# Performance work log

Hardware: AMD Instinct MI355X
Metric: run time of the kernel (lower is better)

Reference implementation:

```python
import jax, jax.numpy as jnp
import numpy as np

B, N, D, E, R = 2, 50000, 128, 500000, 500
LN_EPS = 1e-5


def setup_inputs() -> dict:
    key = jax.random.key(0)
    ks = jax.random.split(key, 12)
    s = 1.0 / np.sqrt(D)
    s2 = 1.0 / np.sqrt(2 * D)
    return {
        "h": jax.random.normal(ks[0], (B, N, D), dtype=jnp.float32),
        "edge_src": jax.random.randint(ks[1], (E,), 0, N),
        "edge_tgt": jax.random.randint(ks[2], (E,), 0, N),
        "edge_rel": jax.random.randint(ks[3], (E,), 0, R),
        "nE": N,
        "msg_W": jax.random.uniform(ks[4], (D, D), jnp.float32, -s, s),
        "rel_emb": jax.random.normal(ks[5], (R, D), dtype=jnp.float32),
        "gate_W": jax.random.uniform(ks[6], (D, D), jnp.float32, -s, s),
        "update_W": jax.random.uniform(ks[7], (2 * D, D), jnp.float32, -s2, s2),
        "update_b": jax.random.uniform(ks[8], (D,), jnp.float32, -s2, s2),
        "ln_gamma": jnp.ones((D,), jnp.float32),
        "ln_beta": jnp.zeros((D,), jnp.float32),
    }


def reference(h, edge_src, edge_tgt, edge_rel, nE, msg_W, rel_emb, gate_W,
              update_W, update_b, ln_gamma, ln_beta):
    r = rel_emb[edge_rel]                      # [E, D]
    h_src = h[:, edge_src]                     # [B, E, D] gather
    gate = jax.nn.sigmoid(h_src @ gate_W)      # [B, E, D]
    msg = (h_src @ msg_W) * r[None] * gate     # [B, E, D]
    # scatter_add over target nodes
    h_agg = jnp.zeros((h.shape[0], nE, h.shape[2]), h.dtype)
    h_agg = h_agg.at[:, edge_tgt].add(msg)     # [B, N, D]
    upd = jnp.concatenate([h, h_agg], axis=-1) @ update_W + update_b
    x = h + jax.nn.relu(upd)
    mu = jnp.mean(x, axis=-1, keepdims=True)
    var = jnp.var(x, axis=-1, keepdims=True)
    h_new = (x - mu) * jax.lax.rsqrt(var + LN_EPS) * ln_gamma + ln_beta
    return h_new
```

## Files before the change

### kernel.cpp

```cpp
#include <hip/hip_runtime.h>

#define DD 128
#define NN 50000
#define BB 2
#define EE 500000
#define LN_EPS 1e-5f

typedef __attribute__((ext_vector_type(8))) short bf16x8;
typedef __attribute__((ext_vector_type(4))) float f32x4;

union FragU { unsigned short u[8]; unsigned int q[4]; bf16x8 v; };

__device__ __forceinline__ unsigned short f2bf(float x) {
  union { float f; unsigned u; } v; v.f = x;
  unsigned r = (v.u + 0x7FFFu + ((v.u >> 16) & 1u)) >> 16;
  return (unsigned short)r;
}
__device__ __forceinline__ float bfbits(short s) {
  union { unsigned u; float f; } v;
  v.u = ((unsigned)(unsigned short)s) << 16;
  return v.f;
}
__device__ __forceinline__ float sigmoidf(float x) {
  return 1.0f / (1.0f + __expf(-x));
}

__device__ __forceinline__ void stage16(const void* g, void* l) {
  __builtin_amdgcn_global_load_lds(
      (const __attribute__((address_space(1))) unsigned int*)g,
      (__attribute__((address_space(3))) unsigned int*)l, 16, 0, 0);
}

__global__ __launch_bounds__(256) void k_prep(
    const float* __restrict__ rel_emb, unsigned short* __restrict__ relb,
    int* __restrict__ deg)
{
  const int id = blockIdx.x * 256 + threadIdx.x;
  if (id < 500 * DD / 2) {
    const float a = rel_emb[2 * id];
    const float b = rel_emb[2 * id + 1];
    *(unsigned int*)&relb[2 * id] =
        (unsigned int)f2bf(a) | ((unsigned int)f2bf(b) << 16);
  }
  if (id < NN) deg[id] = 0;
}

__global__ __launch_bounds__(256) void k_node(
    const float* __restrict__ h, const float* __restrict__ gate_W,
    const float* __restrict__ msg_W, unsigned short* __restrict__ P, int BN)
{
  __shared__ float Hs[3][2048];

  const int t    = threadIdx.x;
  const int lane = t & 63;
  const int n16  = lane & 15;
  const int quad = lane >> 4;
  const int wave = t >> 6;

  FragU ag[2][4], am[2][4];
#pragma unroll
  for (int fi = 0; fi < 2; fi++) {
    const int frow = (wave + fi * 4) * 16 + n16;
#pragma unroll
    for (int ks = 0; ks < 4; ks++) {
      const int k0 = ks * 32 + quad * 8;
#pragma unroll
      for (int e = 0; e < 8; e++) {
        ag[fi][ks].u[e] = f2bf(gate_W[(size_t)(k0 + e) * DD + frow]);
        am[fi][ks].u[e] = f2bf(msg_W[(size_t)(k0 + e) * DD + frow]);
      }
    }
  }

  const int sr = t >> 5, sc = t & 31;
  const size_t g0 = (size_t)sr * 512 +
                    (size_t)((((sc & 24) | ((sc & 7) ^ (sr & 7)))) << 4);

  const int nT    = BN >> 4;
  const int gstep = gridDim.x;
  const int bid   = blockIdx.x;
  const char* hB  = (const char*)h;

#define NSTAGE(slot, tl)                                                     \
  do {                                                                       \
    const char* gb = hB + ((size_t)(tl) << 13);                              \
    char* lb = (char*)&Hs[slot][0];                                          \
    stage16(gb + g0, lb + t * 16);                                           \
    stage16(gb + g0 + 4096, lb + 4096 + t * 16);                             \
  } while (0)

  if (bid < nT)         NSTAGE(0, bid);
  if (bid + gstep < nT) NSTAGE(1, bid + gstep);

  int s = 0;
  for (int tile = bid; tile < nT; tile += gstep) {
    asm volatile("s_waitcnt vmcnt(2)" ::: "memory");
    __builtin_amdgcn_s_barrier();
    asm volatile("" ::: "memory");
    __builtin_amdgcn_sched_barrier(0);

    const float* hs = &Hs[s][0];
    bf16x8 bfr[4];
#pragma unroll
    for (int ks = 0; ks < 4; ks++) {
      const int cc = ks * 8 + quad * 2;
      const int w0 = (cc & 24) | ((cc & 7) ^ (n16 & 7));
      const int w1 = ((cc + 1) & 24) | (((cc + 1) & 7) ^ (n16 & 7));
      const float4 x0 = *(const float4*)(hs + n16 * 128 + w0 * 4);
      const float4 x1 = *(const float4*)(hs + n16 * 128 + w1 * 4);
      FragU f;
      f.u[0] = f2bf(x0.x); f.u[1] = f2bf(x0.y);
      f.u[2] = f2bf(x0.z); f.u[3] = f2bf(x0.w);
      f.u[4] = f2bf(x1.x); f.u[5] = f2bf(x1.y);
      f.u[6] = f2bf(x1.z); f.u[7] = f2bf(x1.w);
      bfr[ks] = f.v;
    }

    f32x4 accg[2], accm[2];
#pragma unroll
    for (int fi = 0; fi < 2; fi++) { accg[fi] = (f32x4)0.f; accm[fi] = (f32x4)0.f; }

#pragma unroll
    for (int fi = 0; fi < 2; fi++)
#pragma unroll
      for (int ks = 0; ks < 4; ks++) {
        accg[fi] = __builtin_amdgcn_mfma_f32_16x16x32_bf16(ag[fi][ks].v, bfr[ks], accg[fi], 0, 0, 0);
        accm[fi] = __builtin_amdgcn_mfma_f32_16x16x32_bf16(am[fi][ks].v, bfr[ks], accm[fi], 0, 0, 0);
      }

    const int b    = (tile * 16 >= NN) ? 1 : 0;
    const int node = tile * 16 + n16 - b * NN;
    unsigned short* Pr = P + (size_t)node * 256 + b * 128;
#pragma unroll
    for (int fi = 0; fi < 2; fi++) {
      const int ft = wave + fi * 4;
      const float v0 = accm[fi][0] * sigmoidf(accg[fi][0]);
      const float v1 = accm[fi][1] * sigmoidf(accg[fi][1]);
      const float v2 = accm[fi][2] * sigmoidf(accg[fi][2]);
      const float v3 = accm[fi][3] * sigmoidf(accg[fi][3]);
      uint2 o;
      o.x = (unsigned int)f2bf(v0) | ((unsigned int)f2bf(v1) << 16);
      o.y = (unsigned int)f2bf(v2) | ((unsigned int)f2bf(v3) << 16);
      *(uint2*)(Pr + ft * 16 + quad * 4) = o;
    }

    asm volatile("" ::: "memory");
    if (tile + 2 * gstep < nT) {
      int s2 = s + 2; if (s2 >= 3) s2 -= 3;
      NSTAGE(s2, tile + 2 * gstep);
    }
    s = (s + 1 >= 3) ? 0 : s + 1;
  }
#undef NSTAGE
}

__global__ __launch_bounds__(256) void k_hist(
    const int* __restrict__ etgt, int* __restrict__ deg)
{
  const int e = blockIdx.x * 256 + threadIdx.x;
  if (e < EE) atomicAdd(&deg[etgt[e]], 1);
}

__global__ __launch_bounds__(256) void k_scan_block(
    const int* __restrict__ deg, int* __restrict__ rstart,
    int* __restrict__ bsum, int N)
{
  __shared__ int s[256];
  const int i = blockIdx.x * 256 + threadIdx.x;
  const int v = (i < N) ? deg[i] : 0;
  s[threadIdx.x] = v;
  __syncthreads();
#pragma unroll
  for (int off = 1; off < 256; off <<= 1) {
    const int tv = (threadIdx.x >= off) ? s[threadIdx.x - off] : 0;
    __syncthreads();
    s[threadIdx.x] += tv;
    __syncthreads();
  }
  if (i < N) rstart[i] = s[threadIdx.x] - v;
  if (threadIdx.x == 255) bsum[blockIdx.x] = s[255];
}

__global__ __launch_bounds__(256) void k_scan_small(
    int* __restrict__ bsum, int* __restrict__ boff, int nb)
{
  __shared__ int s[256];
  const int v = (threadIdx.x < nb) ? bsum[threadIdx.x] : 0;
  s[threadIdx.x] = v;
  __syncthreads();
#pragma unroll
  for (int off = 1; off < 256; off <<= 1) {
    const int tv = (threadIdx.x >= off) ? s[threadIdx.x - off] : 0;
    __syncthreads();
    s[threadIdx.x] += tv;
    __syncthreads();
  }
  if (threadIdx.x < nb) boff[threadIdx.x] = s[threadIdx.x] - v;
}

__global__ __launch_bounds__(256) void k_add_off(
    int* __restrict__ rstart, const int* __restrict__ boff,
    int* __restrict__ cur, int N)
{
  const int i = blockIdx.x * 256 + threadIdx.x;
  if (i < N) {
    const int v = rstart[i] + boff[blockIdx.x];
    rstart[i] = v;
    cur[i] = v;
  }
}

__global__ __launch_bounds__(256) void k_fill(
    const int* __restrict__ esrc, const int* __restrict__ etgt,
    const int* __restrict__ erel, int* __restrict__ cur,
    int* __restrict__ packed)
{
  const int e = blockIdx.x * 256 + threadIdx.x;
  if (e < EE) {
    const int pos = atomicAdd(&cur[etgt[e]], 1);
    packed[pos] = esrc[e] | (erel[e] << 16);
  }
}

__global__ __launch_bounds__(256) void k_agg(
    const unsigned short* __restrict__ P, const unsigned short* __restrict__ relb,
    const int* __restrict__ rstart, const int* __restrict__ packed,
    unsigned short* __restrict__ h_agg)
{
  const int node = blockIdx.x * 4 + (threadIdx.x >> 6);
  if (node >= NN) return;
  const int lane = threadIdx.x & 63;
  const int half = lane >> 5;
  const int c8   = (lane & 31) * 8;
  const int rc   = c8 & 127;

  const int beg = rstart[node];
  const int end = (node == NN - 1) ? EE : rstart[node + 1];

  float acc[8];
#pragma unroll
  for (int i = 0; i < 8; i++) acc[i] = 0.f;

  int j = beg + half;
  for (; j + 2 < end; j += 4) {
    const int p0 = packed[j];
    const int p1 = packed[j + 2];
    const bf16x8 pv0 = *(const bf16x8*)(P + (size_t)(p0 & 0xFFFF) * 256 + c8);
    const bf16x8 rv0 = *(const bf16x8*)(relb + (size_t)(p0 >> 16) * DD + rc);
    const bf16x8 pv1 = *(const bf16x8*)(P + (size_t)(p1 & 0xFFFF) * 256 + c8);
    const bf16x8 rv1 = *(const bf16x8*)(relb + (size_t)(p1 >> 16) * DD + rc);
#pragma unroll
    for (int i = 0; i < 8; i++) {
      acc[i] += bfbits(pv0[i]) * bfbits(rv0[i]);
      acc[i] += bfbits(pv1[i]) * bfbits(rv1[i]);
    }
  }
  for (; j < end; j += 2) {
    const int p0 = packed[j];
    const bf16x8 pv0 = *(const bf16x8*)(P + (size_t)(p0 & 0xFFFF) * 256 + c8);
    const bf16x8 rv0 = *(const bf16x8*)(relb + (size_t)(p0 >> 16) * DD + rc);
#pragma unroll
    for (int i = 0; i < 8; i++) acc[i] += bfbits(pv0[i]) * bfbits(rv0[i]);
  }

#pragma unroll
  for (int i = 0; i < 8; i++) acc[i] += __shfl_xor(acc[i], 32, 64);

  if (half == 0) {
    uint4 o;
    o.x = (unsigned int)f2bf(acc[0]) | ((unsigned int)f2bf(acc[1]) << 16);
    o.y = (unsigned int)f2bf(acc[2]) | ((unsigned int)f2bf(acc[3]) << 16);
    o.z = (unsigned int)f2bf(acc[4]) | ((unsigned int)f2bf(acc[5]) << 16);
    o.w = (unsigned int)f2bf(acc[6]) | ((unsigned int)f2bf(acc[7]) << 16);
    *(uint4*)(h_agg + (size_t)node * 256 + c8) = o;
  }
}

__global__ __launch_bounds__(256) void k_update_ln(
    const float* __restrict__ h, const unsigned short* __restrict__ h_agg,
    const float* __restrict__ upd_W, const float* __restrict__ upd_b,
    const float* __restrict__ gamma, const float* __restrict__ beta,
    float* __restrict__ out, int BN)
{
  __shared__ float Us[3][3072];
  __shared__ float Rs[4][16], Rq[4][16];

  const int t    = threadIdx.x;
  const int lane = t & 63;
  const int n16  = lane & 15;
  const int quad = lane >> 4;
  const int wave = t >> 6;

  FragU aw[2][8];
#pragma unroll
  for (int fi = 0; fi < 2; fi++) {
    const int frow = (wave + fi * 4) * 16 + n16;
#pragma unroll
    for (int ks = 0; ks < 8; ks++) {
      const int k0 = ks * 32 + quad * 8;
#pragma unroll
      for (int e = 0; e < 8; e++)
        aw[fi][ks].u[e] = f2bf(upd_W[(size_t)(k0 + e) * DD + frow]);
    }
  }

  float4 bv[2], gv[2], btv[2];
#pragma unroll
  for (int fi = 0; fi < 2; fi++) {
    const int f0 = (wave + fi * 4) * 16 + quad * 4;
    bv[fi]  = *(const float4*)(upd_b + f0);
    gv[fi]  = *(const float4*)(gamma + f0);
    btv[fi] = *(const float4*)(beta + f0);
  }

  const int sr = t >> 5, sc = t & 31;
  const size_t g0 = (size_t)sr * 512 +
                    (size_t)((((sc & 24) | ((sc & 7) ^ (sr & 7)))) << 4);
  const int ar = t >> 4, ac = t & 15;
  const size_t ga0 = (size_t)ar * 512 +
                     (size_t)((((ac & 8) | ((ac & 7) ^ (ar & 7)))) << 4);

  const int nT    = BN >> 4;
  const int gstep = gridDim.x;
  const int bid   = blockIdx.x;
  const char* hB  = (const char*)h;
  const char* aB  = (const char*)h_agg;

#define USTAGE(slot, tl)                                                     \
  do {                                                                       \
    const char* gb = hB + ((size_t)(tl) << 13);                              \
    char* lb = (char*)&Us[slot][0];                                          \
    stage16(gb + g0, lb + t * 16);                                           \
    stage16(gb + g0 + 4096, lb + 4096 + t * 16);                             \
    const int bb = ((tl) * 16 >= NN) ? 1 : 0;                                \
    const size_t node0 = (size_t)(tl) * 16 - (size_t)bb * NN;                \
    stage16(aB + (node0 << 9) + ((size_t)bb << 8) + ga0, lb + 8192 + t * 16);\
  } while (0)

  if (bid < nT)         USTAGE(0, bid);
  if (bid + gstep < nT) USTAGE(1, bid + gstep);

  int s = 0;
  for (int tile = bid; tile < nT; tile += gstep) {
    asm volatile("s_waitcnt vmcnt(3)" ::: "memory");
    __builtin_amdgcn_s_barrier();
    asm volatile("" ::: "memory");
    __builtin_amdgcn_sched_barrier(0);

    const float* hs = &Us[s][0];
    const unsigned short* ha = (const unsigned short*)(hs + 2048);

    bf16x8 bfr[8];
#pragma unroll
    for (int ks = 0; ks < 4; ks++) {
      const int cc = ks * 8 + quad * 2;
      const int w0 = (cc & 24) | ((cc & 7) ^ (n16 & 7));
      const int w1 = ((cc + 1) & 24) | (((cc + 1) & 7) ^ (n16 & 7));
      const float4 x0 = *(const float4*)(hs + n16 * 128 + w0 * 4);
      const float4 x1 = *(const float4*)(hs + n16 * 128 + w1 * 4);
      FragU f;
      f.u[0] = f2bf(x0.x); f.u[1] = f2bf(x0.y);
      f.u[2] = f2bf(x0.z); f.u[3] = f2bf(x0.w);
      f.u[4] = f2bf(x1.x); f.u[5] = f2bf(x1.y);
      f.u[6] = f2bf(x1.z); f.u[7] = f2bf(x1.w);
      bfr[ks] = f.v;
    }
#pragma unroll
    for (int ks = 0; ks < 4; ks++) {
      const int c  = ks * 4 + quad;
      const int wc = (c & 8) | ((c & 7) ^ (n16 & 7));
      bfr[4 + ks] = *(const bf16x8*)(ha + n16 * 128 + wc * 8);
    }

    f32x4 acc[2];
#pragma unroll
    for (int fi = 0; fi < 2; fi++) acc[fi] = (f32x4)0.f;
#pragma unroll
    for (int fi = 0; fi < 2; fi++)
#pragma unroll
      for (int ks = 0; ks < 8; ks++)
        acc[fi] = __builtin_amdgcn_mfma_f32_16x16x32_bf16(aw[fi][ks].v, bfr[ks], acc[fi], 0, 0, 0);

    float xv[2][4];
    float p1 = 0.f, p2 = 0.f;
#pragma unroll
    for (int fi = 0; fi < 2; fi++) {
      const int ft = wave + fi * 4;
      const int cr = ft * 4 + quad;
      const int wr = (cr & 24) | ((cr & 7) ^ (n16 & 7));
      const float4 hv = *(const float4*)(hs + n16 * 128 + wr * 4);
      xv[fi][0] = hv.x + fmaxf(acc[fi][0] + bv[fi].x, 0.f);
      xv[fi][1] = hv.y + fmaxf(acc[fi][1] + bv[fi].y, 0.f);
      xv[fi][2] = hv.z + fmaxf(acc[fi][2] + bv[fi].z, 0.f);
      xv[fi][3] = hv.w + fmaxf(acc[fi][3] + bv[fi].w, 0.f);
#pragma unroll
      for (int r = 0; r < 4; r++) { p1 += xv[fi][r]; p2 += xv[fi][r] * xv[fi][r]; }
    }
    p1 += __shfl_xor(p1, 16, 64); p2 += __shfl_xor(p2, 16, 64);
    p1 += __shfl_xor(p1, 32, 64); p2 += __shfl_xor(p2, 32, 64);
    if (quad == 0) { Rs[wave][n16] = p1; Rq[wave][n16] = p2; }
    asm volatile("s_waitcnt lgkmcnt(0)" ::: "memory");
    __builtin_amdgcn_s_barrier();
    asm volatile("" ::: "memory");
    const float sA = Rs[0][n16] + Rs[1][n16] + Rs[2][n16] + Rs[3][n16];
    const float sB = Rq[0][n16] + Rq[1][n16] + Rq[2][n16] + Rq[3][n16];

    const float mu   = sA * (1.0f / DD);
    const float var  = sB * (1.0f / DD) - mu * mu;
    const float rstd = rsqrtf(var + LN_EPS);

    const size_t nrow = (size_t)tile * 16 + n16;
#pragma unroll
    for (int fi = 0; fi < 2; fi++) {
      const int f0 = (wave + fi * 4) * 16 + quad * 4;
      float4 o;
      o.x = (xv[fi][0] - mu) * rstd * gv[fi].x + btv[fi].x;
      o.y = (xv[fi][1] - mu) * rstd * gv[fi].y + btv[fi].y;
      o.z = (xv[fi][2] - mu) * rstd * gv[fi].z + btv[fi].z;
      o.w = (xv[fi][3] - mu) * rstd * gv[fi].w + btv[fi].w;
      *(float4*)(out + nrow * DD + f0) = o;
    }

    asm volatile("" ::: "memory");
    if (tile + 2 * gstep < nT) {
      int s2 = s + 2; if (s2 >= 3) s2 -= 3;
      USTAGE(s2, tile + 2 * gstep);
    }
    s = (s + 1 >= 3) ? 0 : s + 1;
  }
#undef USTAGE
}

extern "C" void kernel_launch(void* const* d_in, const int* in_sizes, int n_in,
                              void* d_out, int out_size, void* d_ws, size_t ws_size,
                              hipStream_t stream) {
  const float* h       = (const float*)d_in[0];
  const int*   esrc    = (const int*)d_in[1];
  const int*   etgt    = (const int*)d_in[2];
  const int*   erel    = (const int*)d_in[3];
  const float* msg_W   = (const float*)d_in[5];
  const float* rel_emb = (const float*)d_in[6];
  const float* gate_W  = (const float*)d_in[7];
  const float* upd_W   = (const float*)d_in[8];
  const float* upd_b   = (const float*)d_in[9];
  const float* gamma   = (const float*)d_in[10];
  const float* beta    = (const float*)d_in[11];
  float*       out     = (float*)d_out;

  const int BN = in_sizes[0] / DD;

  unsigned short* P     = (unsigned short*)d_ws;
  unsigned short* h_agg = P + (size_t)NN * 256;
  unsigned short* relb  = h_agg + (size_t)NN * 256;
  int* deg    = (int*)(relb + 500 * DD);
  int* rstart = deg + NN;
  int* cur    = rstart + NN;
  int* bsum   = cur + NN;
  int* boff   = bsum + 256;
  int* packed = boff + 256;

  const int nbN = (NN + 255) / 256;
  const int nbE = (EE + 255) / 256;

  k_prep<<<nbN, 256, 0, stream>>>(rel_emb, relb, deg);

  k_node<<<512, 256, 0, stream>>>(h, gate_W, msg_W, P, BN);

  k_hist<<<nbE, 256, 0, stream>>>(etgt, deg);
  k_scan_block<<<nbN, 256, 0, stream>>>(deg, rstart, bsum, NN);
  k_scan_small<<<1, 256, 0, stream>>>(bsum, boff, nbN);
  k_add_off<<<nbN, 256, 0, stream>>>(rstart, boff, cur, NN);
  k_fill<<<nbE, 256, 0, stream>>>(esrc, etgt, erel, cur, packed);

  k_agg<<<(NN + 3) / 4, 256, 0, stream>>>(P, relb, rstart, packed, h_agg);

  k_update_ln<<<512, 256, 0, stream>>>(h, h_agg, upd_W, upd_b,
                                       gamma, beta, out, BN);
}
```

Measured before the change: 253.0 us.

## Fuse CSR build and aggregation into one cooperative persistent kernel

Replaces the six small graph kernels (prep, histogram, two scans, offset add, fill, aggregate) with a single cooperative kernel of 1024 blocks that separates the phases with grid-wide syncs. The aim is to remove per-kernel launch overhead and tail gaps between the many tiny dependent launches. In exchange it adds grid.sync cost, runs the aggregation as a grid-stride loop over nodes with fewer resident waves, and relies on all 1024 blocks being co-resident for the cooperative launch to succeed.

```diff
diff --git a/kernel.cpp b/kernel.cpp
--- a/kernel.cpp
+++ b/kernel.cpp
@@ -1,4 +1,7 @@
 #include <hip/hip_runtime.h>
+#include <hip/hip_cooperative_groups.h>
+
+namespace cg = cooperative_groups;
 
 #define DD 128
 #define NN 50000
@@ -29,20 +32,6 @@
   __builtin_amdgcn_global_load_lds(
       (const __attribute__((address_space(1))) unsigned int*)g,
       (__attribute__((address_space(3))) unsigned int*)l, 16, 0, 0);
-}
-
-__global__ __launch_bounds__(256) void k_prep(
-    const float* __restrict__ rel_emb, unsigned short* __restrict__ relb,
-    int* __restrict__ deg)
-{
-  const int id = blockIdx.x * 256 + threadIdx.x;
-  if (id < 500 * DD / 2) {
-    const float a = rel_emb[2 * id];
-    const float b = rel_emb[2 * id + 1];
-    *(unsigned int*)&relb[2 * id] =
-        (unsigned int)f2bf(a) | ((unsigned int)f2bf(b) << 16);
-  }
-  if (id < NN) deg[id] = 0;
 }
 
 __global__ __launch_bounds__(256) void k_node(
@@ -154,125 +143,128 @@
 #undef NSTAGE
 }
 
-__global__ __launch_bounds__(256) void k_hist(
-    const int* __restrict__ etgt, int* __restrict__ deg)
+__global__ __launch_bounds__(256, 4) void k_graph(
+    const int* __restrict__ esrc, const int* __restrict__ etgt,
+    const int* __restrict__ erel, const float* __restrict__ rel_emb,
+    unsigned short* __restrict__ relb, int* __restrict__ deg,
+    int* __restrict__ rstart, int* __restrict__ cur,
+    int* __restrict__ bsum, int* __restrict__ boff,
+    int* __restrict__ packed, const unsigned short* __restrict__ P,
+    unsigned short* __restrict__ h_agg)
 {
-  const int e = blockIdx.x * 256 + threadIdx.x;
-  if (e < EE) atomicAdd(&deg[etgt[e]], 1);
-}
-
-__global__ __launch_bounds__(256) void k_scan_block(
-    const int* __restrict__ deg, int* __restrict__ rstart,
-    int* __restrict__ bsum, int N)
-{
+  cg::grid_group grid = cg::this_grid();
   __shared__ int s[256];
-  const int i = blockIdx.x * 256 + threadIdx.x;
-  const int v = (i < N) ? deg[i] : 0;
-  s[threadIdx.x] = v;
-  __syncthreads();
-#pragma unroll
-  for (int off = 1; off < 256; off <<= 1) {
-    const int tv = (threadIdx.x >= off) ? s[threadIdx.x - off] : 0;
+
+  const int t    = threadIdx.x;
+  const int gtid = blockIdx.x * 256 + t;
+  const int gsz  = gridDim.x * 256;
+  const int nbN  = (NN + 255) / 256;
+
+  for (int i = gtid; i < NN; i += gsz) deg[i] = 0;
+  for (int i = gtid; i < 500 * 64; i += gsz) {
+    const float a = rel_emb[2 * i];
+    const float b = rel_emb[2 * i + 1];
+    *(unsigned int*)&relb[2 * i] =
+        (unsigned int)f2bf(a) | ((unsigned int)f2bf(b) << 16);
+  }
+  grid.sync();
+
+  for (int e = gtid; e < EE; e += gsz) atomicAdd(&deg[etgt[e]], 1);
+  grid.sync();
+
+  for (int c = blockIdx.x; c < nbN; c += gridDim.x) {
+    const int i = c * 256 + t;
+    const int v = (i < NN) ? deg[i] : 0;
+    s[t] = v;
     __syncthreads();
-    s[threadIdx.x] += tv;
+#pragma unroll
+    for (int off = 1; off < 256; off <<= 1) {
+      const int tv = (t >= off) ? s[t - off] : 0;
+      __syncthreads();
+      s[t] += tv;
+      __syncthreads();
+    }
+    if (i < NN) rstart[i] = s[t] - v;
+    if (t == 255) bsum[c] = s[255];
+  }
+  grid.sync();
+
+  if (blockIdx.x == 0) {
+    const int v = (t < nbN) ? bsum[t] : 0;
+    s[t] = v;
     __syncthreads();
-  }
-  if (i < N) rstart[i] = s[threadIdx.x] - v;
-  if (threadIdx.x == 255) bsum[blockIdx.x] = s[255];
-}
-
-__global__ __launch_bounds__(256) void k_scan_small(
-    int* __restrict__ bsum, int* __restrict__ boff, int nb)
-{
-  __shared__ int s[256];
-  const int v = (threadIdx.x < nb) ? bsum[threadIdx.x] : 0;
-  s[threadIdx.x] = v;
-  __syncthreads();
-#pragma unroll
-  for (int off = 1; off < 256; off <<= 1) {
-    const int tv = (threadIdx.x >= off) ? s[threadIdx.x - off] : 0;
-    __syncthreads();
-    s[threadIdx.x] += tv;
-    __syncthreads();
-  }
-  if (threadIdx.x < nb) boff[threadIdx.x] = s[threadIdx.x] - v;
-}
-
-__global__ __launch_bounds__(256) void k_add_off(
-    int* __restrict__ rstart, const int* __restrict__ boff,
-    int* __restrict__ cur, int N)
-{
-  const int i = blockIdx.x * 256 + threadIdx.x;
-  if (i < N) {
-    const int v = rstart[i] + boff[blockIdx.x];
+#pragma unroll
+    for (int off = 1; off < 256; off <<= 1) {
+      const int tv = (t >= off) ? s[t - off] : 0;
+      __syncthreads();
+      s[t] += tv;
+      __syncthreads();
+    }
+    if (t < nbN) boff[t] = s[t] - v;
+  }
+  grid.sync();
+
+  for (int i = gtid; i < NN; i += gsz) {
+    const int v = rstart[i] + boff[i >> 8];
     rstart[i] = v;
     cur[i] = v;
   }
-}
-
-__global__ __launch_bounds__(256) void k_fill(
-    const int* __restrict__ esrc, const int* __restrict__ etgt,
-    const int* __restrict__ erel, int* __restrict__ cur,
-    int* __restrict__ packed)
-{
-  const int e = blockIdx.x * 256 + threadIdx.x;
-  if (e < EE) {
+  grid.sync();
+
+  for (int e = gtid; e < EE; e += gsz) {
     const int pos = atomicAdd(&cur[etgt[e]], 1);
     packed[pos] = esrc[e] | (erel[e] << 16);
   }
-}
-
-__global__ __launch_bounds__(256) void k_agg(
-    const unsigned short* __restrict__ P, const unsigned short* __restrict__ relb,
-    const int* __restrict__ rstart, const int* __restrict__ packed,
-    unsigned short* __restrict__ h_agg)
-{
-  const int node = blockIdx.x * 4 + (threadIdx.x >> 6);
-  if (node >= NN) return;
-  const int lane = threadIdx.x & 63;
+  grid.sync();
+
+  const int lane = t & 63;
   const int half = lane >> 5;
   const int c8   = (lane & 31) * 8;
   const int rc   = c8 & 127;
-
-  const int beg = rstart[node];
-  const int end = (node == NN - 1) ? EE : rstart[node + 1];
-
-  float acc[8];
-#pragma unroll
-  for (int i = 0; i < 8; i++) acc[i] = 0.f;
-
-  int j = beg + half;
-  for (; j + 2 < end; j += 4) {
-    const int p0 = packed[j];
-    const int p1 = packed[j + 2];
-    const bf16x8 pv0 = *(const bf16x8*)(P + (size_t)(p0 & 0xFFFF) * 256 + c8);
-    const bf16x8 rv0 = *(const bf16x8*)(relb + (size_t)(p0 >> 16) * DD + rc);
-    const bf16x8 pv1 = *(const bf16x8*)(P + (size_t)(p1 & 0xFFFF) * 256 + c8);
-    const bf16x8 rv1 = *(const bf16x8*)(relb + (size_t)(p1 >> 16) * DD + rc);
-#pragma unroll
-    for (int i = 0; i < 8; i++) {
-      acc[i] += bfbits(pv0[i]) * bfbits(rv0[i]);
-      acc[i] += bfbits(pv1[i]) * bfbits(rv1[i]);
-    }
-  }
-  for (; j < end; j += 2) {
-    const int p0 = packed[j];
-    const bf16x8 pv0 = *(const bf16x8*)(P + (size_t)(p0 & 0xFFFF) * 256 + c8);
-    const bf16x8 rv0 = *(const bf16x8*)(relb + (size_t)(p0 >> 16) * DD + rc);
-#pragma unroll
-    for (int i = 0; i < 8; i++) acc[i] += bfbits(pv0[i]) * bfbits(rv0[i]);
-  }
-
-#pragma unroll
-  for (int i = 0; i < 8; i++) acc[i] += __shfl_xor(acc[i], 32, 64);
-
-  if (half == 0) {
-    uint4 o;
-    o.x = (unsigned int)f2bf(acc[0]) | ((unsigned int)f2bf(acc[1]) << 16);
-    o.y = (unsigned int)f2bf(acc[2]) | ((unsigned int)f2bf(acc[3]) << 16);
-    o.z = (unsigned int)f2bf(acc[4]) | ((unsigned int)f2bf(acc[5]) << 16);
-    o.w = (unsigned int)f2bf(acc[6]) | ((unsigned int)f2bf(acc[7]) << 16);
-    *(uint4*)(h_agg + (size_t)node * 256 + c8) = o;
+  const int wv   = blockIdx.x * 4 + (t >> 6);
+  const int nw   = gridDim.x * 4;
+
+  for (int node = wv; node < NN; node += nw) {
+    const int beg = rstart[node];
+    const int end = (node == NN - 1) ? EE : rstart[node + 1];
+
+    float acc[8];
+#pragma unroll
+    for (int i = 0; i < 8; i++) acc[i] = 0.f;
+
+    int j = beg + half;
+    for (; j + 2 < end; j += 4) {
+      const int p0 = packed[j];
+      const int p1 = packed[j + 2];
+      const bf16x8 pv0 = *(const bf16x8*)(P + (size_t)(p0 & 0xFFFF) * 256 + c8);
+      const bf16x8 rv0 = *(const bf16x8*)(relb + (size_t)(p0 >> 16) * DD + rc);
+      const bf16x8 pv1 = *(const bf16x8*)(P + (size_t)(p1 & 0xFFFF) * 256 + c8);
+      const bf16x8 rv1 = *(const bf16x8*)(relb + (size_t)(p1 >> 16) * DD + rc);
+#pragma unroll
+      for (int i = 0; i < 8; i++) {
+        acc[i] += bfbits(pv0[i]) * bfbits(rv0[i]);
+        acc[i] += bfbits(pv1[i]) * bfbits(rv1[i]);
+      }
+    }
+    for (; j < end; j += 2) {
+      const int p0 = packed[j];
+      const bf16x8 pv0 = *(const bf16x8*)(P + (size_t)(p0 & 0xFFFF) * 256 + c8);
+      const bf16x8 rv0 = *(const bf16x8*)(relb + (size_t)(p0 >> 16) * DD + rc);
+#pragma unroll
+      for (int i = 0; i < 8; i++) acc[i] += bfbits(pv0[i]) * bfbits(rv0[i]);
+    }
+
+#pragma unroll
+    for (int i = 0; i < 8; i++) acc[i] += __shfl_xor(acc[i], 32, 64);
+
+    if (half == 0) {
+      uint4 o;
+      o.x = (unsigned int)f2bf(acc[0]) | ((unsigned int)f2bf(acc[1]) << 16);
+      o.y = (unsigned int)f2bf(acc[2]) | ((unsigned int)f2bf(acc[3]) << 16);
+      o.z = (unsigned int)f2bf(acc[4]) | ((unsigned int)f2bf(acc[5]) << 16);
+      o.w = (unsigned int)f2bf(acc[6]) | ((unsigned int)f2bf(acc[7]) << 16);
+      *(uint4*)(h_agg + (size_t)node * 256 + c8) = o;
+    }
   }
 }
 
@@ -459,20 +451,16 @@
   int* boff   = bsum + 256;
   int* packed = boff + 256;
 
-  const int nbN = (NN + 255) / 256;
-  const int nbE = (EE + 255) / 256;
-
-  k_prep<<<nbN, 256, 0, stream>>>(rel_emb, relb, deg);
-
   k_node<<<512, 256, 0, stream>>>(h, gate_W, msg_W, P, BN);
 
-  k_hist<<<nbE, 256, 0, stream>>>(etgt, deg);
-  k_scan_block<<<nbN, 256, 0, stream>>>(deg, rstart, bsum, NN);
-  k_scan_small<<<1, 256, 0, stream>>>(bsum, boff, nbN);
-  k_add_off<<<nbN, 256, 0, stream>>>(rstart, boff, cur, NN);
-  k_fill<<<nbE, 256, 0, stream>>>(esrc, etgt, erel, cur, packed);
-
-  k_agg<<<(NN + 3) / 4, 256, 0, stream>>>(P, relb, rstart, packed, h_agg);
+  {
+    void* ka[] = { (void*)&esrc, (void*)&etgt, (void*)&erel, (void*)&rel_emb,
+                   (void*)&relb, (void*)&deg, (void*)&rstart, (void*)&cur,
+                   (void*)&bsum, (void*)&boff, (void*)&packed, (void*)&P,
+                   (void*)&h_agg };
+    hipLaunchCooperativeKernel((void*)k_graph, dim3(1024), dim3(256),
+                               ka, 0, stream);
+  }
 
   k_update_ln<<<512, 256, 0, stream>>>(h, h_agg, upd_W, upd_b,
                                        gamma, beta, out, BN);
```

Result: slower. 874.6 us (+245.7%).
